# Kernel optimization log

Measured on AMD Instinct MI355X. Metric: run time of the kernel, lower is better.

Reference implementation:

```python
import jax, jax.numpy as jnp
import numpy as np

N = 8192
NFEAT = 512
NHID = 512
NCLASS = 8
EPS = 1e-9
ADJ_P = 0.01  # edge density


def setup_inputs() -> dict:
    key = jax.random.key(0)
    ks = jax.random.split(key, 16)
    adj = (jax.random.uniform(ks[0], (N, N)) < ADJ_P).astype(jnp.float32)
    x = jax.random.normal(ks[1], (N, NFEAT), dtype=jnp.float32)
    s_in = 1.0 / np.sqrt(NFEAT)
    s_h = 1.0 / np.sqrt(NHID)
    return {
        "adj": adj,
        "x": x,
        "gcn1_W": jax.random.normal(ks[2], (NFEAT, NHID), jnp.float32) * s_in,
        "gcn1_b": jnp.zeros((NHID,), jnp.float32),
        "Qw": jax.random.normal(ks[3], (NHID, NHID), jnp.float32) * s_h,
        "Qb": jnp.zeros((NHID,), jnp.float32),
        "Kw": jax.random.normal(ks[4], (NHID, NHID), jnp.float32) * s_h,
        "Kb": jnp.zeros((NHID,), jnp.float32),
        "Vw": jax.random.normal(ks[5], (NHID, NHID), jnp.float32) * s_h,
        "Vb": jnp.zeros((NHID,), jnp.float32),
        "ln_g": jnp.ones((NHID,), jnp.float32),
        "ln_b": jnp.zeros((NHID,), jnp.float32),
        "gcn2_W": jax.random.normal(ks[6], (NHID, NCLASS), jnp.float32) * s_h,
        "gcn2_b": jnp.zeros((NCLASS,), jnp.float32),
    }


def _gcn_norm(a):
    # symmetric degree normalization D^{-1/2} A D^{-1/2}, degrees = row sums
    d_inv_sqrt = jax.lax.rsqrt(a.sum(axis=1) + EPS)  # [N]
    return d_inv_sqrt[:, None] * a * d_inv_sqrt[None, :]


def _layer_norm(x, g, b):
    mu = x.mean(axis=-1, keepdims=True)
    var = x.var(axis=-1, keepdims=True)
    return (x - mu) * jax.lax.rsqrt(var + 1e-5) * g + b


def reference(adj, x, gcn1_W, gcn1_b, Qw, Qb, Kw, Kb, Vw, Vb, ln_g, ln_b, gcn2_W, gcn2_b):
    # GraphConvolution: adj @ (x W) + b, then ReLU
    h = jax.nn.relu(adj @ (x @ gcn1_W) + gcn1_b)  # [N, NHID]
    Qh = h @ Qw + Qb
    Kh = h @ Kw + Kb
    Vh = h @ Vw + Vb
    # adjacency-masked dense scores (multiplicative mask, as in original)
    A_tilde = adj * (Qh @ Kh.T)  # [N, N]
    attention = jax.nn.softmax(A_tilde, axis=1)
    X_tilde = _gcn_norm(attention) @ Vh  # [N, NHID]
    X_tilde = _layer_norm(X_tilde, ln_g, ln_b)
    z = adj @ (X_tilde @ gcn2_W) + gcn2_b  # [N, NCLASS]
    return jax.nn.softmax(z, axis=1)
```

## Files before the change

kernel.cpp:

```cpp
#include <hip/hip_runtime.h>
#include <math.h>

#define N_NODES 8192
#define NFEAT 512
#define NHID 512
#define NCLASS 8
#define RCAP 192
#define KB_SPLIT 1536
#define KA_SPLIT 1024
#define CANDCAP 64
#define FILTER_MARGIN 96.0f

__device__ inline ushort f2bf(float f) {
  uint32_t u = __float_as_uint(f);
  uint32_t r = u + 0x7fffu + ((u >> 16) & 1u);
  return (ushort)(r >> 16);
}
__device__ inline float bf2f(ushort h) { return __uint_as_float(((uint32_t)h) << 16); }

__global__ __launch_bounds__(256) void build_ell(const float* __restrict__ adj,
                                                 int* __restrict__ colidx,
                                                 int* __restrict__ deg) {
  int row = blockIdx.x;
  __shared__ int cnt;
  __shared__ int cols[RCAP];
  if (threadIdx.x == 0) cnt = 0;
  __syncthreads();
  const float4* arow = (const float4*)(adj + (size_t)row * N_NODES);
  for (int i = threadIdx.x; i < N_NODES / 4; i += 256) {
    float4 v = arow[i];
    int base = i * 4;
    if (v.x > 0.5f) { int p = atomicAdd(&cnt, 1); if (p < RCAP) cols[p] = base; }
    if (v.y > 0.5f) { int p = atomicAdd(&cnt, 1); if (p < RCAP) cols[p] = base + 1; }
    if (v.z > 0.5f) { int p = atomicAdd(&cnt, 1); if (p < RCAP) cols[p] = base + 2; }
    if (v.w > 0.5f) { int p = atomicAdd(&cnt, 1); if (p < RCAP) cols[p] = base + 3; }
  }
  __syncthreads();
  int d = cnt < RCAP ? cnt : RCAP;
  if (threadIdx.x == 0) deg[row] = d;
  for (int i = threadIdx.x; i < d; i += 256) colidx[(size_t)row * RCAP + i] = cols[i];
}

__global__ void transpose512(const float* __restrict__ in, float* __restrict__ out) {
  __shared__ float tile[32][33];
  int x = blockIdx.x * 32 + threadIdx.x;
  int y0 = blockIdx.y * 32;
  for (int i = threadIdx.y; i < 32; i += 8)
    tile[i][threadIdx.x] = in[(size_t)(y0 + i) * 512 + x];
  __syncthreads();
  int xo = blockIdx.y * 32 + threadIdx.x;
  int yo0 = blockIdx.x * 32;
  for (int i = threadIdx.y; i < 32; i += 8)
    out[(size_t)(yo0 + i) * 512 + xo] = tile[threadIdx.x][i];
}

__global__ __launch_bounds__(256) void sgemm64x128(const float* __restrict__ A,
                                                   const float* __restrict__ B,
                                                   float* __restrict__ C,
                                                   int M, int Nn, int K, int ldc) {
  __shared__ float As[16][68];
  __shared__ float Bs[16][132];
  const int tid = threadIdx.x;
  const int bm = blockIdx.y * 64, bn = blockIdx.x * 128;
  const int tx = tid & 15, ty = tid >> 4;
  const int arow = tid >> 2, acol = (tid & 3) << 2;
  const int brow = tid >> 4, bcol = (tid & 15) << 2;
  float acc[4][8];
#pragma unroll
  for (int i = 0; i < 4; ++i)
#pragma unroll
    for (int j = 0; j < 8; ++j) acc[i][j] = 0.f;
  const float* Ap = A + (size_t)(bm + arow) * K + acol;
  const float* Bp = B + (size_t)brow * Nn + bn + bcol;
// ... 169 lines not shown
    }
    if (Tsum && col >= 512) {
      csum += __shfl_xor(csum, 16, 64);
      csum += __shfl_xor(csum, 32, 64);
      if (q == 0) atomicAdd(&Tsum[col - 512], csum);
    }
  }
}

__global__ __launch_bounds__(64) void bias_prep(const float* __restrict__ Qw, const float* __restrict__ Kw,
                                                const float* __restrict__ Qb, const float* __restrict__ Kb,
                                                float* __restrict__ u, float* __restrict__ w,
                                                float* __restrict__ cbuf) {
  int k = blockIdx.x;
  int lane = threadIdx.x;
  if (k == NHID) {
    float s = 0.f;
    for (int j = lane; j < NHID; j += 64) s = fmaf(Qb[j], Kb[j], s);
#pragma unroll
    for (int o = 32; o > 0; o >>= 1) s += __shfl_down(s, o, 64);
    if (lane == 0) cbuf[0] = s;
    return;
  }
  float su = 0.f, sw = 0.f;
  for (int j = lane; j < NHID; j += 64) {
    su = fmaf(Qw[(size_t)k * NHID + j], Kb[j], su);
    sw = fmaf(Kw[(size_t)k * NHID + j], Qb[j], sw);
  }
#pragma unroll
  for (int o = 32; o > 0; o >>= 1) { su += __shfl_down(su, o, 64); sw += __shfl_down(sw, o, 64); }
  if (lane == 0) { u[k] = su; w[k] = sw; }
}

__global__ __launch_bounds__(128) void spmm_fused(const float* __restrict__ xW,
                                                  const int* __restrict__ colidx,
                                                  const int* __restrict__ deg,
                                                  const float* __restrict__ b1,
                                                  const float* __restrict__ u, const float* __restrict__ w,
                                                  float* __restrict__ h, ushort* __restrict__ Hs,
                                                  float* __restrict__ a_vec, float* __restrict__ b_vec) {
  __shared__ int scols[RCAP];
  __shared__ float ra[2], rb[2];
  int row = blockIdx.x, t = threadIdx.x;
  int d = deg[row];
  for (int i = t; i < d; i += 128) scols[i] = colidx[(size_t)row * RCAP + i];
  __syncthreads();
  float4 acc = make_float4(0.f, 0.f, 0.f, 0.f);
  int e = 0;
  for (; e + 8 <= d; e += 8) {
    float4 v0 = ((const float4*)(xW + (size_t)scols[e + 0] * NHID))[t];
    float4 v1 = ((const float4*)(xW + (size_t)scols[e + 1] * NHID))[t];
    float4 v2 = ((const float4*)(xW + (size_t)scols[e + 2] * NHID))[t];
    float4 v3 = ((const float4*)(xW + (size_t)scols[e + 3] * NHID))[t];
    float4 v4 = ((const float4*)(xW + (size_t)scols[e + 4] * NHID))[t];
    float4 v5 = ((const float4*)(xW + (size_t)scols[e + 5] * NHID))[t];
    float4 v6 = ((const float4*)(xW + (size_t)scols[e + 6] * NHID))[t];
    float4 v7 = ((const float4*)(xW + (size_t)scols[e + 7] * NHID))[t];
    acc.x += ((v0.x + v1.x) + (v2.x + v3.x)) + ((v4.x + v5.x) + (v6.x + v7.x));
    acc.y += ((v0.y + v1.y) + (v2.y + v3.y)) + ((v4.y + v5.y) + (v6.y + v7.y));
    acc.z += ((v0.z + v1.z) + (v2.z + v3.z)) + ((v4.z + v5.z) + (v6.z + v7.z));
    acc.w += ((v0.w + v1.w) + (v2.w + v3.w)) + ((v4.w + v5.w) + (v6.w + v7.w));
  }
  for (; e < d; ++e) {
    float4 v = ((const float4*)(xW + (size_t)scols[e] * NHID))[t];
    acc.x += v.x; acc.y += v.y; acc.z += v.z; acc.w += v.w;
  }
  float4 bv = ((const float4*)b1)[t];
  float4 o = make_float4(fmaxf(acc.x + bv.x, 0.f), fmaxf(acc.y + bv.y, 0.f),
                         fmaxf(acc.z + bv.z, 0.f), fmaxf(acc.w + bv.w, 0.f));
  ((float4*)(h + (size_t)row * NHID))[t] = o;
  ushort4 hi, lo;
  hi.x = f2bf(o.x); hi.y = f2bf(o.y); hi.z = f2bf(o.z); hi.w = f2bf(o.w);
  lo.x = f2bf(o.x - bf2f(hi.x)); lo.y = f2bf(o.y - bf2f(hi.y));
  lo.z = f2bf(o.z - bf2f(hi.z)); lo.w = f2bf(o.w - bf2f(hi.w));
  ushort* hr = Hs + (size_t)row * KA_SPLIT;
  ((ushort4*)hr)[t] = hi;
  ((ushort4*)(hr + 512))[t] = lo;
  float4 uv = ((const float4*)u)[t], wv4 = ((const float4*)w)[t];
  float sa = fmaf(o.x, uv.x, fmaf(o.y, uv.y, fmaf(o.z, uv.z, o.w * uv.w)));
  float sb = fmaf(o.x, wv4.x, fmaf(o.y, wv4.y, fmaf(o.z, wv4.z, o.w * wv4.w)));
  int wv = t >> 6, lane = t & 63;
#pragma unroll
  for (int off = 32; off > 0; off >>= 1) { sa += __shfl_down(sa, off, 64); sb += __shfl_down(sb, off, 64); }
  if (lane == 0) { ra[wv] = sa; rb[wv] = sb; }
  __syncthreads();
  if (t == 0) { a_vec[row] = ra[0] + ra[1]; b_vec[row] = rb[0] + rb[1]; }
}

__global__ __launch_bounds__(256) void score2_agg_ln(
    const float* __restrict__ G, int ldg, const float* __restrict__ h,
    const ushort* __restrict__ Hs, const int* __restrict__ colidx, const int* __restrict__ deg,
    const float* __restrict__ a_vec, const float* __restrict__ b_vec,
    const float* __restrict__ cbuf, const float* __restrict__ Vh, int ldv,
    const float* __restrict__ T, const float* __restrict__ lng,
    const float* __restrict__ lnb, float* __restrict__ Xt) {
  __shared__ int scols[4][RCAP];
  __shared__ float sbv[4][RCAP];
  __shared__ float sv[4][RCAP];
  __shared__ int cand[4][CANDCAP];
  __shared__ int ccnt[4];
  int t = threadIdx.x, wv = t >> 6, lane = t & 63;
  int row = blockIdx.x * 4 + wv;
  int d = deg[row];
  int q = lane >> 4, u = lane & 15;
  if (lane == 0) ccnt[wv] = 0;
  float4 ga4[4][2];
  const float4* Gr4 = (const float4*)(G + (size_t)row * ldg);
#pragma unroll
  for (int it2 = 0; it2 < 4; ++it2) {
    ga4[it2][0] = Gr4[it2 * 32 + 2 * u];
    ga4[it2][1] = Gr4[it2 * 32 + 2 * u + 1];
  }
  for (int i = lane; i < d; i += 64) {
    int c = colidx[(size_t)row * RCAP + i];
    scols[wv][i] = c;
    sbv[wv][i] = b_vec[c];
  }
  __syncthreads();
  for (int e0 = 0; e0 < d; e0 += 4) {
    int e = e0 + q;
    bool act = e < d;
    int col = scols[wv][act ? e : 0];
    const uint4* hr = (const uint4*)(Hs + (size_t)col * KA_SPLIT);
    float s_a = 0.f, s_b = 0.f;
#pragma unroll
    for (int it2 = 0; it2 < 4; ++it2) {
      uint4 p = hr[it2 * 16 + u];
      float4 g0 = ga4[it2][0], g1 = ga4[it2][1];
      s_a = fmaf(__uint_as_float(p.x << 16), g0.x, s_a);
      s_a = fmaf(__uint_as_float(p.x & 0xffff0000u), g0.y, s_a);
      s_a = fmaf(__uint_as_float(p.y << 16), g0.z, s_a);
      s_a = fmaf(__uint_as_float(p.y & 0xffff0000u), g0.w, s_a);
      s_b = fmaf(__uint_as_float(p.z << 16), g1.x, s_b);
      s_b = fmaf(__uint_as_float(p.z & 0xffff0000u), g1.y, s_b);
      s_b = fmaf(__uint_as_float(p.w << 16), g1.z, s_b);
      s_b = fmaf(__uint_as_float(p.w & 0xffff0000u), g1.w, s_b);
    }
    float s = s_a + s_b;
    s += __shfl_down(s, 8, 16);
    s += __shfl_down(s, 4, 16);
    s += __shfl_down(s, 2, 16);
    s += __shfl_down(s, 1, 16);
    if (u == 0 && act) sv[wv][e] = s + sbv[wv][e];
  }
  __syncthreads();
  float fm = -1e30f;
  for (int i = lane; i < d; i += 64) fm = fmaxf(fm, sv[wv][i]);
#pragma unroll
  for (int o = 32; o > 0; o >>= 1) fm = fmaxf(fm, __shfl_xor(fm, o, 64));
  for (int i = lane; i < d; i += 64) {
    if (sv[wv][i] >= fm - FILTER_MARGIN) {
      int p = atomicAdd(&ccnt[wv], 1);
      if (p < CANDCAP) cand[wv][p] = i;
    }
  }
  __syncthreads();
  int nc = ccnt[wv];
  bool ovf = nc > CANDCAP;
  if (ovf) nc = d;
  float ai = a_vec[row] + cbuf[0];
  for (int c0 = 0; c0 < nc; c0 += 4) {
    int idx = c0 + q;
    bool act = idx < nc;
    int e = act ? (ovf ? idx : cand[wv][idx]) : 0;
    int col = scols[wv][e];
    const float4* hr = (const float4*)(h + (size_t)col * NHID);
    float s_a = 0.f, s_b = 0.f;
#pragma unroll
    for (int it2 = 0; it2 < 4; ++it2) {
      float4 h0 = hr[it2 * 32 + 2 * u], h1 = hr[it2 * 32 + 2 * u + 1];
      float4 g0 = ga4[it2][0], g1 = ga4[it2][1];
      s_a = fmaf(h0.x, g0.x, s_a); s_a = fmaf(h0.y, g0.y, s_a);
      s_a = fmaf(h0.z, g0.z, s_a); s_a = fmaf(h0.w, g0.w, s_a);
      s_b = fmaf(h1.x, g1.x, s_b); s_b = fmaf(h1.y, g1.y, s_b);
      s_b = fmaf(h1.z, g1.z, s_b); s_b = fmaf(h1.w, g1.w, s_b);
    }
    float s = s_a + s_b;
    s += __shfl_down(s, 8, 16);
    s += __shfl_down(s, 4, 16);
    s += __shfl_down(s, 2, 16);
    s += __shfl_down(s, 1, 16);
    if (u == 0 && act) sv[wv][e] = s + ai + sbv[wv][e];
  }
  __syncthreads();
  float m = 0.f;
  for (int i = lane; i < nc; i += 64) {
    int e = ovf ? i : cand[wv][i];
    m = fmaxf(m, sv[wv][e]);
  }
#pragma unroll
  for (int o = 32; o > 0; o >>= 1) m = fmaxf(m, __shfl_xor(m, o, 64));
  float ssum = 0.f;
  for (int i = lane; i < nc; i += 64) {
    int e = ovf ? i : cand[wv][i];
    float ex = expf(sv[wv][e] - m);
    sv[wv][e] = ex;
    ssum += ex;
  }
#pragma unroll
  for (int o = 32; o > 0; o >>= 1) ssum += __shfl_xor(ssum, o, 64);
  float em = expf(-m);
  float inv = 1.f / (ssum + (float)(N_NODES - d) * em);
  float ci = em * inv;
  __syncthreads();
  float4 a0 = make_float4(0.f, 0.f, 0.f, 0.f), a1 = a0;
  for (int i = 0; i < nc; ++i) {
    int e = ovf ? i : cand[wv][i];
    float we = sv[wv][e] * inv;
    if (we > 1e-12f) {
      const float4* vr = (const float4*)(Vh + (size_t)scols[wv][e] * ldv);
      float4 v0 = vr[lane * 2], v1 = vr[lane * 2 + 1];
      a0.x = fmaf(we, v0.x, a0.x); a0.y = fmaf(we, v0.y, a0.y);
      a0.z = fmaf(we, v0.z, a0.z); a0.w = fmaf(we, v0.w, a0.w);
      a1.x = fmaf(we, v1.x, a1.x); a1.y = fmaf(we, v1.y, a1.y);
      a1.z = fmaf(we, v1.z, a1.z); a1.w = fmaf(we, v1.w, a1.w);
    }
  }
  float4 t0 = ((const float4*)T)[lane * 2], t1 = ((const float4*)T)[lane * 2 + 1];
  a0.x = fmaf(ci, t0.x, a0.x); a0.y = fmaf(ci, t0.y, a0.y);
  a0.z = fmaf(ci, t0.z, a0.z); a0.w = fmaf(ci, t0.w, a0.w);
  a1.x = fmaf(ci, t1.x, a1.x); a1.y = fmaf(ci, t1.y, a1.y);
  a1.z = fmaf(ci, t1.z, a1.z); a1.w = fmaf(ci, t1.w, a1.w);
  float s1 = ((a0.x + a0.y) + (a0.z + a0.w)) + ((a1.x + a1.y) + (a1.z + a1.w));
  float s2 = ((a0.x * a0.x + a0.y * a0.y) + (a0.z * a0.z + a0.w * a0.w)) +
             ((a1.x * a1.x + a1.y * a1.y) + (a1.z * a1.z + a1.w * a1.w));
#pragma unroll
  for (int o = 32; o > 0; o >>= 1) { s1 += __shfl_xor(s1, o, 64); s2 += __shfl_xor(s2, o, 64); }
  float mu = s1 * (1.f / NHID);
  float var = s2 * (1.f / NHID) - mu * mu;
  float rstd = rsqrtf(var + 1e-5f);
  float4 g0 = ((const float4*)lng)[lane * 2], g1 = ((const float4*)lng)[lane * 2 + 1];
  float4 b0 = ((const float4*)lnb)[lane * 2], b1 = ((const float4*)lnb)[lane * 2 + 1];
  float4 o0, o1;
  o0.x = (a0.x - mu) * rstd * g0.x + b0.x;
  o0.y = (a0.y - mu) * rstd * g0.y + b0.y;
  o0.z = (a0.z - mu) * rstd * g0.z + b0.z;
  o0.w = (a0.w - mu) * rstd * g0.w + b0.w;
  o1.x = (a1.x - mu) * rstd * g1.x + b1.x;
  o1.y = (a1.y - mu) * rstd * g1.y + b1.y;
  o1.z = (a1.z - mu) * rstd * g1.z + b1.z;
  o1.w = (a1.w - mu) * rstd * g1.w + b1.w;
  float4* xr = (float4*)(Xt + (size_t)row * NHID);
  xr[lane * 2] = o0;
  xr[lane * 2 + 1] = o1;
}

__global__ __launch_bounds__(256) void xt_w2(const float* __restrict__ Xt, const float* __restrict__ W2,
                                             float* __restrict__ Y) {
  __shared__ float w2s[NHID * NCLASS];
  int t = threadIdx.x;
  for (int i = t; i < NHID * NCLASS; i += 256) w2s[i] = W2[i];
  __syncthreads();
  int wv = t >> 6, lane = t & 63;
  int row = blockIdx.x * 4 + wv;
  const float4* xr = (const float4*)(Xt + (size_t)row * NHID);
  float4 x0 = xr[lane * 2], x1 = xr[lane * 2 + 1];
  float xv[8] = {x0.x, x0.y, x0.z, x0.w, x1.x, x1.y, x1.z, x1.w};
  float acc[NCLASS];
#pragma unroll
  for (int c = 0; c < NCLASS; ++c) acc[c] = 0.f;
#pragma unroll
  for (int kk = 0; kk < 8; ++kk) {
    int k = lane * 8 + kk;
#pragma unroll
    for (int c = 0; c < NCLASS; ++c) acc[c] = fmaf(xv[kk], w2s[k * NCLASS + c], acc[c]);
  }
#pragma unroll
  for (int c = 0; c < NCLASS; ++c)
#pragma unroll
    for (int o = 32; o > 0; o >>= 1) acc[c] += __shfl_down(acc[c], o, 64);
  if (lane == 0) {
    *(float4*)(Y + (size_t)row * NCLASS) = make_float4(acc[0], acc[1], acc[2], acc[3]);
    *(float4*)(Y + (size_t)row * NCLASS + 4) = make_float4(acc[4], acc[5], acc[6], acc[7]);
  }
}

__global__ __launch_bounds__(256) void final_spmm_softmax(const float* __restrict__ Y,
                                                          const int* __restrict__ colidx,
                                                          const int* __restrict__ deg,
                                                          const float* __restrict__ b2,
                                                          float* __restrict__ out) {
  int t = threadIdx.x;
  int wv = t >> 6, lane = t & 63;
  int row = blockIdx.x * 4 + wv;
  int d = deg[row];
  const int* cols = colidx + (size_t)row * RCAP;
  float acc[8];
#pragma unroll
  for (int c = 0; c < 8; ++c) acc[c] = 0.f;
  for (int e = lane; e < d; e += 64) {
    int col = cols[e];
    const float4* yr = (const float4*)(Y + (size_t)col * 8);
    float4 y0 = yr[0], y1 = yr[1];
    acc[0] += y0.x; acc[1] += y0.y; acc[2] += y0.z; acc[3] += y0.w;
    acc[4] += y1.x; acc[5] += y1.y; acc[6] += y1.z; acc[7] += y1.w;
  }
#pragma unroll
  for (int c = 0; c < 8; ++c)
#pragma unroll
    for (int o = 32; o > 0; o >>= 1) acc[c] += __shfl_down(acc[c], o, 64);
  if (lane == 0) {
    float z[8];
    float m = -1e30f;
#pragma unroll
    for (int c = 0; c < 8; ++c) { z[c] = acc[c] + b2[c]; m = fmaxf(m, z[c]); }
    float s = 0.f;
#pragma unroll
    for (int c = 0; c < 8; ++c) { z[c] = expf(z[c] - m); s += z[c]; }
    float inv = 1.f / s;
    *(float4*)(out + (size_t)row * 8) = make_float4(z[0] * inv, z[1] * inv, z[2] * inv, z[3] * inv);
    *(float4*)(out + (size_t)row * 8 + 4) = make_float4(z[4] * inv, z[5] * inv, z[6] * inv, z[7] * inv);
  }
}

extern "C" void kernel_launch(void* const* d_in, const int* in_sizes, int n_in,
                              void* d_out, int out_size, void* d_ws, size_t ws_size,
                              hipStream_t stream) {
  const float* adj = (const float*)d_in[0];
  const float* x = (const float*)d_in[1];
  const float* W1 = (const float*)d_in[2];
  const float* b1 = (const float*)d_in[3];
  const float* Qw = (const float*)d_in[4];
  const float* Qb = (const float*)d_in[5];
  const float* Kw = (const float*)d_in[6];
  const float* Kb = (const float*)d_in[7];
  const float* Vw = (const float*)d_in[8];
  const float* Vb = (const float*)d_in[9];
  const float* ln_g = (const float*)d_in[10];
  const float* ln_b = (const float*)d_in[11];
  const float* W2 = (const float*)d_in[12];
  const float* b2 = (const float*)d_in[13];
  float* out = (float*)d_out;

  char* ws = (char*)d_ws;
  size_t off = 0;
  auto alloc = [&](size_t bytes) -> void* {
    void* p = ws + off;
    off = (off + bytes + 255) & ~(size_t)255;
    return p;
  };
  int* colidx = (int*)alloc((size_t)N_NODES * RCAP * 4);
  int* deg = (int*)alloc((size_t)N_NODES * 4);
  float* bufA = (float*)alloc((size_t)N_NODES * NHID * 4);
  float* bufB = (float*)alloc((size_t)N_NODES * NHID * 4);
  float* GVh = (float*)alloc((size_t)N_NODES * 1024 * 4);
  ushort* Xs = (ushort*)alloc((size_t)N_NODES * KA_SPLIT * 2);
  ushort* Hs = (ushort*)alloc((size_t)N_NODES * KA_SPLIT * 2);
  ushort* W1ts = (ushort*)alloc((size_t)512 * KB_SPLIT * 2);
  ushort* Bcts = (ushort*)alloc((size_t)1024 * KB_SPLIT * 2);
  float* KwT = (float*)alloc((size_t)512 * 512 * 4);
  float* Mmat = (float*)alloc((size_t)512 * 512 * 4);
  float* bcat = (float*)alloc((size_t)1024 * 4);
  float* a_vec = (float*)alloc((size_t)N_NODES * 4);
  float* b_vec = (float*)alloc((size_t)N_NODES * 4);
  float* u_vec = (float*)alloc((size_t)NHID * 4);
  float* w_vec = (float*)alloc((size_t)NHID * 4);
  float* cbuf = (float*)alloc(256);
  float* T = (float*)alloc((size_t)NHID * 4);
  float* Y = (float*)alloc((size_t)N_NODES * NCLASS * 4);
  (void)in_sizes; (void)n_in; (void)out_size; (void)ws_size;

  build_ell<<<N_NODES, 256, 0, stream>>>(adj, colidx, deg);
  transpose512<<<dim3(16, 16), dim3(32, 8), 0, stream>>>(Kw, KwT);
  bias_prep<<<NHID + 1, 64, 0, stream>>>(Qw, Kw, Qb, Kb, u_vec, w_vec, cbuf);
  sgemm64x128<<<dim3(4, 8), 256, 0, stream>>>(Qw, KwT, Mmat, 512, 512, 512, 512);
  split_a2<<<(N_NODES * 128) / 256, 256, 0, stream>>>(x, Xs);
  split_bt<<<(512 * 384) / 256, 256, 0, stream>>>(W1, W1ts, 512);
  mfma_gemm_bt<<<dim3(4, 64), 256, 0, stream>>>(Xs, W1ts, nullptr, bufA, 512, nullptr);
  spmm_fused<<<N_NODES, 128, 0, stream>>>(bufA, colidx, deg, b1, u_vec, w_vec, bufB, Hs, a_vec, b_vec);
  split_bt_cat<<<(1024 * 384) / 256, 256, 0, stream>>>(Mmat, Vw, Bcts);
  prep_misc<<<6, 256, 0, stream>>>(Vb, bcat, T);
  mfma_gemm_bt<<<dim3(8, 64), 256, 0, stream>>>(Hs, Bcts, bcat, GVh, 1024, T);
  score2_agg_ln<<<N_NODES / 4, 256, 0, stream>>>(GVh, 1024, bufB, Hs, colidx, deg, a_vec, b_vec,
                                                 cbuf, GVh + 512, 1024, T, ln_g, ln_b, bufA);
  xt_w2<<<N_NODES / 4, 256, 0, stream>>>(bufA, W2, Y);
  final_spmm_softmax<<<N_NODES / 4, 256, 0, stream>>>(Y, colidx, deg, b2, out);
}
```

Before: 763.5 us.

## Segment ELL columns into four column-range passes for cache locality; fuse W2 projection

Splits each row's neighbor list into four column segments of 2048 nodes, then runs the SpMM and the bf16 score filter as four passes, one segment each. Every pass only gathers rows from a 2048-node window, so the gathered working set can stay cache-resident. The xt_w2 kernel is folded into the attention/layernorm kernel, which also removes the Xt round-trip. Costs are more kernel launches, partial-sum read/write of h across the passes, a new score buffer, and a fixed 64-per-segment cap that can drop edges on dense segments.

```diff
diff --git a/kernel.cpp b/kernel.cpp
--- a/kernel.cpp
+++ b/kernel.cpp
@@ -5,7 +5,10 @@
 #define NFEAT 512
 #define NHID 512
 #define NCLASS 8
-#define RCAP 192
+#define NSEG 4
+#define SEGW 2048
+#define SEGCAP 64
+#define SLOTS 256
 #define KB_SPLIT 1536
 #define KA_SPLIT 1024
 #define CANDCAP 64
@@ -20,25 +23,30 @@
 
 __global__ __launch_bounds__(256) void build_ell(const float* __restrict__ adj,
                                                  int* __restrict__ colidx,
-                                                 int* __restrict__ deg) {
+                                                 int* __restrict__ deg4) {
   int row = blockIdx.x;
-  __shared__ int cnt;
-  __shared__ int cols[RCAP];
-  if (threadIdx.x == 0) cnt = 0;
+  __shared__ int cnt[NSEG];
+  __shared__ int cols[NSEG][SEGCAP];
+  if (threadIdx.x < NSEG) cnt[threadIdx.x] = 0;
   __syncthreads();
   const float4* arow = (const float4*)(adj + (size_t)row * N_NODES);
   for (int i = threadIdx.x; i < N_NODES / 4; i += 256) {
     float4 v = arow[i];
     int base = i * 4;
-    if (v.x > 0.5f) { int p = atomicAdd(&cnt, 1); if (p < RCAP) cols[p] = base; }
-    if (v.y > 0.5f) { int p = atomicAdd(&cnt, 1); if (p < RCAP) cols[p] = base + 1; }
-    if (v.z > 0.5f) { int p = atomicAdd(&cnt, 1); if (p < RCAP) cols[p] = base + 2; }
-    if (v.w > 0.5f) { int p = atomicAdd(&cnt, 1); if (p < RCAP) cols[p] = base + 3; }
-  }
-  __syncthreads();
-  int d = cnt < RCAP ? cnt : RCAP;
-  if (threadIdx.x == 0) deg[row] = d;
-  for (int i = threadIdx.x; i < d; i += 256) colidx[(size_t)row * RCAP + i] = cols[i];
+    if (v.x > 0.5f) { int c = base + 0, s = c >> 11; int p = atomicAdd(&cnt[s], 1); if (p < SEGCAP) cols[s][p] = c; }
+    if (v.y > 0.5f) { int c = base + 1, s = c >> 11; int p = atomicAdd(&cnt[s], 1); if (p < SEGCAP) cols[s][p] = c; }
+    if (v.z > 0.5f) { int c = base + 2, s = c >> 11; int p = atomicAdd(&cnt[s], 1); if (p < SEGCAP) cols[s][p] = c; }
+    if (v.w > 0.5f) { int c = base + 3, s = c >> 11; int p = atomicAdd(&cnt[s], 1); if (p < SEGCAP) cols[s][p] = c; }
+  }
+  __syncthreads();
+  if (threadIdx.x < NSEG) {
+    int c = cnt[threadIdx.x];
+    deg4[row * NSEG + threadIdx.x] = c < SEGCAP ? c : SEGCAP;
+  }
+  for (int s = 0; s < NSEG; ++s) {
+    int d = cnt[s] < SEGCAP ? cnt[s] : SEGCAP;
+    for (int i = threadIdx.x; i < d; i += 256) colidx[(size_t)row * SLOTS + s * SEGCAP + i] = cols[s][i];
+  }
 }
 
 __global__ void transpose512(const float* __restrict__ in, float* __restrict__ out) {
@@ -274,38 +282,42 @@
   if (lane == 0) { u[k] = su; w[k] = sw; }
 }
 
-__global__ __launch_bounds__(128) void spmm_fused(const float* __restrict__ xW,
-                                                  const int* __restrict__ colidx,
-                                                  const int* __restrict__ deg,
-                                                  const float* __restrict__ b1,
-                                                  const float* __restrict__ u, const float* __restrict__ w,
-                                                  float* __restrict__ h, ushort* __restrict__ Hs,
-                                                  float* __restrict__ a_vec, float* __restrict__ b_vec) {
-  __shared__ int scols[RCAP];
+__global__ __launch_bounds__(128) void spmm_pass(const float* __restrict__ xW,
+                                                 const int* __restrict__ colidx,
+                                                 const int* __restrict__ deg4, int seg,
+                                                 const float* __restrict__ b1,
+                                                 const float* __restrict__ u_vec,
+                                                 const float* __restrict__ w_vec,
+                                                 float* __restrict__ h, ushort* __restrict__ Hs,
+                                                 float* __restrict__ a_vec, float* __restrict__ b_vec,
+                                                 int isFinal) {
+  __shared__ int scols[SEGCAP];
   __shared__ float ra[2], rb[2];
   int row = blockIdx.x, t = threadIdx.x;
-  int d = deg[row];
-  for (int i = t; i < d; i += 128) scols[i] = colidx[(size_t)row * RCAP + i];
-  __syncthreads();
-  float4 acc = make_float4(0.f, 0.f, 0.f, 0.f);
+  int d = deg4[row * NSEG + seg];
+  for (int i = t; i < d; i += 128) scols[i] = colidx[(size_t)row * SLOTS + seg * SEGCAP + i];
+  __syncthreads();
+  float4 acc;
+  if (seg == 0) acc = make_float4(0.f, 0.f, 0.f, 0.f);
+  else acc = ((const float4*)(h + (size_t)row * NHID))[t];
   int e = 0;
-  for (; e + 8 <= d; e += 8) {
+  for (; e + 4 <= d; e += 4) {
     float4 v0 = ((const float4*)(xW + (size_t)scols[e + 0] * NHID))[t];
     float4 v1 = ((const float4*)(xW + (size_t)scols[e + 1] * NHID))[t];
     float4 v2 = ((const float4*)(xW + (size_t)scols[e + 2] * NHID))[t];
     float4 v3 = ((const float4*)(xW + (size_t)scols[e + 3] * NHID))[t];
-    float4 v4 = ((const float4*)(xW + (size_t)scols[e + 4] * NHID))[t];
-    float4 v5 = ((const float4*)(xW + (size_t)scols[e + 5] * NHID))[t];
-    float4 v6 = ((const float4*)(xW + (size_t)scols[e + 6] * NHID))[t];
-    float4 v7 = ((const float4*)(xW + (size_t)scols[e + 7] * NHID))[t];
-    acc.x += ((v0.x + v1.x) + (v2.x + v3.x)) + ((v4.x + v5.x) + (v6.x + v7.x));
-    acc.y += ((v0.y + v1.y) + (v2.y + v3.y)) + ((v4.y + v5.y) + (v6.y + v7.y));
-    acc.z += ((v0.z + v1.z) + (v2.z + v3.z)) + ((v4.z + v5.z) + (v6.z + v7.z));
-    acc.w += ((v0.w + v1.w) + (v2.w + v3.w)) + ((v4.w + v5.w) + (v6.w + v7.w));
+    acc.x += (v0.x + v1.x) + (v2.x + v3.x);
+    acc.y += (v0.y + v1.y) + (v2.y + v3.y);
+    acc.z += (v0.z + v1.z) + (v2.z + v3.z);
+    acc.w += (v0.w + v1.w) + (v2.w + v3.w);
   }
   for (; e < d; ++e) {
     float4 v = ((const float4*)(xW + (size_t)scols[e] * NHID))[t];
     acc.x += v.x; acc.y += v.y; acc.z += v.z; acc.w += v.w;
+  }
+  if (!isFinal) {
+    ((float4*)(h + (size_t)row * NHID))[t] = acc;
+    return;
   }
   float4 bv = ((const float4*)b1)[t];
   float4 o = make_float4(fmaxf(acc.x + bv.x, 0.f), fmaxf(acc.y + bv.y, 0.f),
@@ -318,34 +330,27 @@
   ushort* hr = Hs + (size_t)row * KA_SPLIT;
   ((ushort4*)hr)[t] = hi;
   ((ushort4*)(hr + 512))[t] = lo;
-  float4 uv = ((const float4*)u)[t], wv4 = ((const float4*)w)[t];
+  float4 uv = ((const float4*)u_vec)[t], wv4 = ((const float4*)w_vec)[t];
   float sa = fmaf(o.x, uv.x, fmaf(o.y, uv.y, fmaf(o.z, uv.z, o.w * uv.w)));
   float sb = fmaf(o.x, wv4.x, fmaf(o.y, wv4.y, fmaf(o.z, wv4.z, o.w * wv4.w)));
-  int wv = t >> 6, lane = t & 63;
+  int wid = t >> 6, lane = t & 63;
 #pragma unroll
   for (int off = 32; off > 0; off >>= 1) { sa += __shfl_down(sa, off, 64); sb += __shfl_down(sb, off, 64); }
-  if (lane == 0) { ra[wv] = sa; rb[wv] = sb; }
+  if (lane == 0) { ra[wid] = sa; rb[wid] = sb; }
   __syncthreads();
   if (t == 0) { a_vec[row] = ra[0] + ra[1]; b_vec[row] = rb[0] + rb[1]; }
 }
 
-__global__ __launch_bounds__(256) void score2_agg_ln(
-    const float* __restrict__ G, int ldg, const float* __restrict__ h,
-    const ushort* __restrict__ Hs, const int* __restrict__ colidx, const int* __restrict__ deg,
-    const float* __restrict__ a_vec, const float* __restrict__ b_vec,
-    const float* __restrict__ cbuf, const float* __restrict__ Vh, int ldv,
-    const float* __restrict__ T, const float* __restrict__ lng,
-    const float* __restrict__ lnb, float* __restrict__ Xt) {
-  __shared__ int scols[4][RCAP];
-  __shared__ float sbv[4][RCAP];
-  __shared__ float sv[4][RCAP];
-  __shared__ int cand[4][CANDCAP];
-  __shared__ int ccnt[4];
+__global__ __launch_bounds__(256) void filter_pass(const float* __restrict__ G, int ldg,
+                                                   const ushort* __restrict__ Hs,
+                                                   const int* __restrict__ colidx,
+                                                   const int* __restrict__ deg4,
+                                                   const float* __restrict__ b_vec,
+                                                   float* __restrict__ svg, int seg) {
   int t = threadIdx.x, wv = t >> 6, lane = t & 63;
   int row = blockIdx.x * 4 + wv;
-  int d = deg[row];
   int q = lane >> 4, u = lane & 15;
-  if (lane == 0) ccnt[wv] = 0;
+  int d = deg4[row * NSEG + seg];
   float4 ga4[4][2];
   const float4* Gr4 = (const float4*)(G + (size_t)row * ldg);
 #pragma unroll
@@ -353,16 +358,12 @@
     ga4[it2][0] = Gr4[it2 * 32 + 2 * u];
     ga4[it2][1] = Gr4[it2 * 32 + 2 * u + 1];
   }
-  for (int i = lane; i < d; i += 64) {
-    int c = colidx[(size_t)row * RCAP + i];
-    scols[wv][i] = c;
-    sbv[wv][i] = b_vec[c];
-  }
-  __syncthreads();
+  const int* ci = colidx + (size_t)row * SLOTS + seg * SEGCAP;
+  float* so = svg + (size_t)row * SLOTS + seg * SEGCAP;
   for (int e0 = 0; e0 < d; e0 += 4) {
     int e = e0 + q;
     bool act = e < d;
-    int col = scols[wv][act ? e : 0];
+    int col = ci[act ? e : 0];
     const uint4* hr = (const uint4*)(Hs + (size_t)col * KA_SPLIT);
     float s_a = 0.f, s_b = 0.f;
 #pragma unroll
@@ -383,15 +384,56 @@
     s += __shfl_down(s, 4, 16);
     s += __shfl_down(s, 2, 16);
     s += __shfl_down(s, 1, 16);
-    if (u == 0 && act) sv[wv][e] = s + sbv[wv][e];
+    if (u == 0 && act) so[e] = s + b_vec[col];
+  }
+}
+
+__global__ __launch_bounds__(256) void score2_main(
+    const float* __restrict__ G, int ldg, const float* __restrict__ h,
+    const int* __restrict__ colidx, const int* __restrict__ deg4,
+    const float* __restrict__ a_vec, const float* __restrict__ b_vec,
+    const float* __restrict__ cbuf, const float* __restrict__ Vh, int ldv,
+    const float* __restrict__ svg, const float* __restrict__ T,
+    const float* __restrict__ lng, const float* __restrict__ lnb,
+    const float* __restrict__ W2, float* __restrict__ Y) {
+  __shared__ int scols[4][SLOTS];
+  __shared__ float sf[4][SLOTS];
+  __shared__ int cand[4][CANDCAP];
+  __shared__ int ccnt[4];
+  __shared__ float w2s[NHID * NCLASS];
+  int t = threadIdx.x, wv = t >> 6, lane = t & 63;
+  int row = blockIdx.x * 4 + wv;
+  int q = lane >> 4, u = lane & 15;
+  for (int i = t; i < NHID * NCLASS; i += 256) w2s[i] = W2[i];
+  if (lane == 0) ccnt[wv] = 0;
+  int4 dv = ((const int4*)deg4)[row];
+  int dtot = dv.x + dv.y + dv.z + dv.w;
+  for (int i = lane; i < SLOTS; i += 64) {
+    int s = i >> 6, k = i & 63;
+    int ds = (s == 0) ? dv.x : (s == 1) ? dv.y : (s == 2) ? dv.z : dv.w;
+    int c = 0;
+    float f = -1e30f;
+    if (k < ds) {
+      c = colidx[(size_t)row * SLOTS + i];
+      f = svg[(size_t)row * SLOTS + i];
+    }
+    scols[wv][i] = c;
+    sf[wv][i] = f;
+  }
+  float4 ga4[4][2];
+  const float4* Gr4 = (const float4*)(G + (size_t)row * ldg);
+#pragma unroll
+  for (int it2 = 0; it2 < 4; ++it2) {
+    ga4[it2][0] = Gr4[it2 * 32 + 2 * u];
+    ga4[it2][1] = Gr4[it2 * 32 + 2 * u + 1];
   }
   __syncthreads();
   float fm = -1e30f;
-  for (int i = lane; i < d; i += 64) fm = fmaxf(fm, sv[wv][i]);
+  for (int i = lane; i < SLOTS; i += 64) fm = fmaxf(fm, sf[wv][i]);
 #pragma unroll
   for (int o = 32; o > 0; o >>= 1) fm = fmaxf(fm, __shfl_xor(fm, o, 64));
-  for (int i = lane; i < d; i += 64) {
-    if (sv[wv][i] >= fm - FILTER_MARGIN) {
+  for (int i = lane; i < SLOTS; i += 64) {
+    if (sf[wv][i] >= fm - FILTER_MARGIN) {
       int p = atomicAdd(&ccnt[wv], 1);
       if (p < CANDCAP) cand[wv][p] = i;
     }
@@ -399,13 +441,14 @@
   __syncthreads();
   int nc = ccnt[wv];
   bool ovf = nc > CANDCAP;
-  if (ovf) nc = d;
+  if (ovf) nc = SLOTS;
   float ai = a_vec[row] + cbuf[0];
   for (int c0 = 0; c0 < nc; c0 += 4) {
     int idx = c0 + q;
     bool act = idx < nc;
-    int e = act ? (ovf ? idx : cand[wv][idx]) : 0;
-    int col = scols[wv][e];
+    int slot = act ? (ovf ? idx : cand[wv][idx]) : 0;
+    if (ovf && act) act = sf[wv][slot] > -1e29f;
+    int col = scols[wv][slot];
     const float4* hr = (const float4*)(h + (size_t)col * NHID);
     float s_a = 0.f, s_b = 0.f;
 #pragma unroll
@@ -422,35 +465,35 @@
     s += __shfl_down(s, 4, 16);
     s += __shfl_down(s, 2, 16);
     s += __shfl_down(s, 1, 16);
-    if (u == 0 && act) sv[wv][e] = s + ai + sbv[wv][e];
+    if (u == 0 && act) sf[wv][slot] = s + ai + b_vec[col];
   }
   __syncthreads();
   float m = 0.f;
   for (int i = lane; i < nc; i += 64) {
-    int e = ovf ? i : cand[wv][i];
-    m = fmaxf(m, sv[wv][e]);
+    int slot = ovf ? i : cand[wv][i];
+    m = fmaxf(m, sf[wv][slot]);
   }
 #pragma unroll
   for (int o = 32; o > 0; o >>= 1) m = fmaxf(m, __shfl_xor(m, o, 64));
   float ssum = 0.f;
   for (int i = lane; i < nc; i += 64) {
-    int e = ovf ? i : cand[wv][i];
-    float ex = expf(sv[wv][e] - m);
-    sv[wv][e] = ex;
+    int slot = ovf ? i : cand[wv][i];
+    float ex = expf(sf[wv][slot] - m);
+    sf[wv][slot] = ex;
     ssum += ex;
   }
 #pragma unroll
   for (int o = 32; o > 0; o >>= 1) ssum += __shfl_xor(ssum, o, 64);
   float em = expf(-m);
-  float inv = 1.f / (ssum + (float)(N_NODES - d) * em);
+  float inv = 1.f / (ssum + (float)(N_NODES - dtot) * em);
   float ci = em * inv;
   __syncthreads();
   float4 a0 = make_float4(0.f, 0.f, 0.f, 0.f), a1 = a0;
   for (int i = 0; i < nc; ++i) {
-    int e = ovf ? i : cand[wv][i];
-    float we = sv[wv][e] * inv;
+    int slot = ovf ? i : cand[wv][i];
+    float we = sf[wv][slot] * inv;
     if (we > 1e-12f) {
-      const float4* vr = (const float4*)(Vh + (size_t)scols[wv][e] * ldv);
+      const float4* vr = (const float4*)(Vh + (size_t)scols[wv][slot] * ldv);
       float4 v0 = vr[lane * 2], v1 = vr[lane * 2 + 1];
       a0.x = fmaf(we, v0.x, a0.x); a0.y = fmaf(we, v0.y, a0.y);
       a0.z = fmaf(we, v0.z, a0.z); a0.w = fmaf(we, v0.w, a0.w);
@@ -472,70 +515,58 @@
   float var = s2 * (1.f / NHID) - mu * mu;
   float rstd = rsqrtf(var + 1e-5f);
   float4 g0 = ((const float4*)lng)[lane * 2], g1 = ((const float4*)lng)[lane * 2 + 1];
-  float4 b0 = ((const float4*)lnb)[lane * 2], b1 = ((const float4*)lnb)[lane * 2 + 1];
+  float4 b0 = ((const float4*)lnb)[lane * 2], b1v = ((const float4*)lnb)[lane * 2 + 1];
   float4 o0, o1;
   o0.x = (a0.x - mu) * rstd * g0.x + b0.x;
   o0.y = (a0.y - mu) * rstd * g0.y + b0.y;
   o0.z = (a0.z - mu) * rstd * g0.z + b0.z;
   o0.w = (a0.w - mu) * rstd * g0.w + b0.w;
-  o1.x = (a1.x - mu) * rstd * g1.x + b1.x;
-  o1.y = (a1.y - mu) * rstd * g1.y + b1.y;
-  o1.z = (a1.z - mu) * rstd * g1.z + b1.z;
-  o1.w = (a1.w - mu) * rstd * g1.w + b1.w;
-  float4* xr = (float4*)(Xt + (size_t)row * NHID);
-  xr[lane * 2] = o0;
-  xr[lane * 2 + 1] = o1;
-}
-
-__global__ __launch_bounds__(256) void xt_w2(const float* __restrict__ Xt, const float* __restrict__ W2,
-                                             float* __restrict__ Y) {
-  __shared__ float w2s[NHID * NCLASS];
-  int t = threadIdx.x;
-  for (int i = t; i < NHID * NCLASS; i += 256) w2s[i] = W2[i];
-  __syncthreads();
-  int wv = t >> 6, lane = t & 63;
-  int row = blockIdx.x * 4 + wv;
-  const float4* xr = (const float4*)(Xt + (size_t)row * NHID);
-  float4 x0 = xr[lane * 2], x1 = xr[lane * 2 + 1];
-  float xv[8] = {x0.x, x0.y, x0.z, x0.w, x1.x, x1.y, x1.z, x1.w};
-  float acc[NCLASS];
-#pragma unroll
-  for (int c = 0; c < NCLASS; ++c) acc[c] = 0.f;
+  o1.x = (a1.x - mu) * rstd * g1.x + b1v.x;
+  o1.y = (a1.y - mu) * rstd * g1.y + b1v.y;
+  o1.z = (a1.z - mu) * rstd * g1.z + b1v.z;
+  o1.w = (a1.w - mu) * rstd * g1.w + b1v.w;
+  float xv[8] = {o0.x, o0.y, o0.z, o0.w, o1.x, o1.y, o1.z, o1.w};
+  float accc[NCLASS];
+#pragma unroll
+  for (int c = 0; c < NCLASS; ++c) accc[c] = 0.f;
 #pragma unroll
   for (int kk = 0; kk < 8; ++kk) {
     int k = lane * 8 + kk;
 #pragma unroll
-    for (int c = 0; c < NCLASS; ++c) acc[c] = fmaf(xv[kk], w2s[k * NCLASS + c], acc[c]);
+    for (int c = 0; c < NCLASS; ++c) accc[c] = fmaf(xv[kk], w2s[k * NCLASS + c], accc[c]);
   }
 #pragma unroll
   for (int c = 0; c < NCLASS; ++c)
 #pragma unroll
-    for (int o = 32; o > 0; o >>= 1) acc[c] += __shfl_down(acc[c], o, 64);
+    for (int o = 32; o > 0; o >>= 1) accc[c] += __shfl_down(accc[c], o, 64);
   if (lane == 0) {
-    *(float4*)(Y + (size_t)row * NCLASS) = make_float4(acc[0], acc[1], acc[2], acc[3]);
-    *(float4*)(Y + (size_t)row * NCLASS + 4) = make_float4(acc[4], acc[5], acc[6], acc[7]);
+    *(float4*)(Y + (size_t)row * NCLASS) = make_float4(accc[0], accc[1], accc[2], accc[3]);
+    *(float4*)(Y + (size_t)row * NCLASS + 4) = make_float4(accc[4], accc[5], accc[6], accc[7]);
   }
 }
 
 __global__ __launch_bounds__(256) void final_spmm_softmax(const float* __restrict__ Y,
                                                           const int* __restrict__ colidx,
-                                                          const int* __restrict__ deg,
+                                                          const int* __restrict__ deg4,
                                                           const float* __restrict__ b2,
                                                           float* __restrict__ out) {
   int t = threadIdx.x;
   int wv = t >> 6, lane = t & 63;
   int row = blockIdx.x * 4 + wv;
-  int d = deg[row];
-  const int* cols = colidx + (size_t)row * RCAP;
+  int4 dv = ((const int4*)deg4)[row];
   float acc[8];
 #pragma unroll
   for (int c = 0; c < 8; ++c) acc[c] = 0.f;
-  for (int e = lane; e < d; e += 64) {
-    int col = cols[e];
-    const float4* yr = (const float4*)(Y + (size_t)col * 8);
-    float4 y0 = yr[0], y1 = yr[1];
-    acc[0] += y0.x; acc[1] += y0.y; acc[2] += y0.z; acc[3] += y0.w;
-    acc[4] += y1.x; acc[5] += y1.y; acc[6] += y1.z; acc[7] += y1.w;
+  for (int i = lane; i < SLOTS; i += 64) {
+    int s = i >> 6, k = i & 63;
+    int ds = (s == 0) ? dv.x : (s == 1) ? dv.y : (s == 2) ? dv.z : dv.w;
+    if (k < ds) {
+      int col = colidx[(size_t)row * SLOTS + i];
+      const float4* yr = (const float4*)(Y + (size_t)col * 8);
+      float4 y0 = yr[0], y1 = yr[1];
+      acc[0] += y0.x; acc[1] += y0.y; acc[2] += y0.z; acc[3] += y0.w;
+      acc[4] += y1.x; acc[5] += y1.y; acc[6] += y1.z; acc[7] += y1.w;
+    }
   }
 #pragma unroll
   for (int c = 0; c < 8; ++c)
@@ -581,11 +612,12 @@
     off = (off + bytes + 255) & ~(size_t)255;
     return p;
   };
-  int* colidx = (int*)alloc((size_t)N_NODES * RCAP * 4);
-  int* deg = (int*)alloc((size_t)N_NODES * 4);
+  int* colidx = (int*)alloc((size_t)N_NODES * SLOTS * 4);
+  int* deg4 = (int*)alloc((size_t)N_NODES * NSEG * 4);
   float* bufA = (float*)alloc((size_t)N_NODES * NHID * 4);
   float* bufB = (float*)alloc((size_t)N_NODES * NHID * 4);
   float* GVh = (float*)alloc((size_t)N_NODES * 1024 * 4);
+  float* svg = (float*)alloc((size_t)N_NODES * SLOTS * 4);
   ushort* Xs = (ushort*)alloc((size_t)N_NODES * KA_SPLIT * 2);
   ushort* Hs = (ushort*)alloc((size_t)N_NODES * KA_SPLIT * 2);
   ushort* W1ts = (ushort*)alloc((size_t)512 * KB_SPLIT * 2);
@@ -602,19 +634,22 @@
   float* Y = (float*)alloc((size_t)N_NODES * NCLASS * 4);
   (void)in_sizes; (void)n_in; (void)out_size; (void)ws_size;
 
-  build_ell<<<N_NODES, 256, 0, stream>>>(adj, colidx, deg);
+  build_ell<<<N_NODES, 256, 0, stream>>>(adj, colidx, deg4);
   transpose512<<<dim3(16, 16), dim3(32, 8), 0, stream>>>(Kw, KwT);
   bias_prep<<<NHID + 1, 64, 0, stream>>>(Qw, Kw, Qb, Kb, u_vec, w_vec, cbuf);
   sgemm64x128<<<dim3(4, 8), 256, 0, stream>>>(Qw, KwT, Mmat, 512, 512, 512, 512);
   split_a2<<<(N_NODES * 128) / 256, 256, 0, stream>>>(x, Xs);
   split_bt<<<(512 * 384) / 256, 256, 0, stream>>>(W1, W1ts, 512);
   mfma_gemm_bt<<<dim3(4, 64), 256, 0, stream>>>(Xs, W1ts, nullptr, bufA, 512, nullptr);
-  spmm_fused<<<N_NODES, 128, 0, stream>>>(bufA, colidx, deg, b1, u_vec, w_vec, bufB, Hs, a_vec, b_vec);
+  for (int s = 0; s < NSEG; ++s)
+    spmm_pass<<<N_NODES, 128, 0, stream>>>(bufA, colidx, deg4, s, b1, u_vec, w_vec,
+                                           bufB, Hs, a_vec, b_vec, s == NSEG - 1);
   split_bt_cat<<<(1024 * 384) / 256, 256, 0, stream>>>(Mmat, Vw, Bcts);
   prep_misc<<<6, 256, 0, stream>>>(Vb, bcat, T);
   mfma_gemm_bt<<<dim3(8, 64), 256, 0, stream>>>(Hs, Bcts, bcat, GVh, 1024, T);
-  score2_agg_ln<<<N_NODES / 4, 256, 0, stream>>>(GVh, 1024, bufB, Hs, colidx, deg, a_vec, b_vec,
-                                                 cbuf, GVh + 512, 1024, T, ln_g, ln_b, bufA);
-  xt_w2<<<N_NODES / 4, 256, 0, stream>>>(bufA, W2, Y);
-  final_spmm_softmax<<<N_NODES / 4, 256, 0, stream>>>(Y, colidx, deg, b2, out);
-}
+  for (int s = 0; s < NSEG; ++s)
+    filter_pass<<<N_NODES / 4, 256, 0, stream>>>(GVh, 1024, Hs, colidx, deg4, b_vec, svg, s);
+  score2_main<<<N_NODES / 4, 256, 0, stream>>>(GVh, 1024, bufB, colidx, deg4, a_vec, b_vec,
+                                               cbuf, GVh + 512, 1024, svg, T, ln_g, ln_b, W2, Y);
+  final_spmm_softmax<<<N_NODES / 4, 256, 0, stream>>>(Y, colidx, deg4, b2, out);
+}
```

Result: faster. 747.3 us (-2.1%).

## Fuse Xt·W2 into aggregation kernel and batch SpMM rows per block

Applied to the files above, without the earlier changes.

The layer-norm output is multiplied by W2 inside score2_agg_ln, which removes the xt_w2 kernel and the round trip of the full Xt matrix through global memory. The first SpMM now handles 8 rows per block and interleaves their neighbour gathers to expose more memory-level parallelism, at the cost of more registers and shared memory. build_ell's row scan is unrolled with a barrier per iteration. The extra W2 staging adds shared memory to the aggregation kernel, which may lower its occupancy.

```diff
diff --git a/kernel.cpp b/kernel.cpp
--- a/kernel.cpp
+++ b/kernel.cpp
@@ -10,6 +10,7 @@
 #define KA_SPLIT 1024
 #define CANDCAP 64
 #define FILTER_MARGIN 96.0f
+#define SROWS 8
 
 __device__ inline ushort f2bf(float f) {
   uint32_t u = __float_as_uint(f);
@@ -27,15 +28,17 @@
   if (threadIdx.x == 0) cnt = 0;
   __syncthreads();
   const float4* arow = (const float4*)(adj + (size_t)row * N_NODES);
-  for (int i = threadIdx.x; i < N_NODES / 4; i += 256) {
+#pragma unroll
+  for (int it = 0; it < N_NODES / 4 / 256; ++it) {
+    int i = it * 256 + threadIdx.x;
     float4 v = arow[i];
     int base = i * 4;
     if (v.x > 0.5f) { int p = atomicAdd(&cnt, 1); if (p < RCAP) cols[p] = base; }
     if (v.y > 0.5f) { int p = atomicAdd(&cnt, 1); if (p < RCAP) cols[p] = base + 1; }
     if (v.z > 0.5f) { int p = atomicAdd(&cnt, 1); if (p < RCAP) cols[p] = base + 2; }
     if (v.w > 0.5f) { int p = atomicAdd(&cnt, 1); if (p < RCAP) cols[p] = base + 3; }
-  }
-  __syncthreads();
+    __syncthreads();
+  }
   int d = cnt < RCAP ? cnt : RCAP;
   if (threadIdx.x == 0) deg[row] = d;
   for (int i = threadIdx.x; i < d; i += 256) colidx[(size_t)row * RCAP + i] = cols[i];
@@ -274,59 +277,63 @@
   if (lane == 0) { u[k] = su; w[k] = sw; }
 }
 
-__global__ __launch_bounds__(128) void spmm_fused(const float* __restrict__ xW,
-                                                  const int* __restrict__ colidx,
-                                                  const int* __restrict__ deg,
-                                                  const float* __restrict__ b1,
-                                                  const float* __restrict__ u, const float* __restrict__ w,
-                                                  float* __restrict__ h, ushort* __restrict__ Hs,
-                                                  float* __restrict__ a_vec, float* __restrict__ b_vec) {
-  __shared__ int scols[RCAP];
+__global__ __launch_bounds__(128) void spmm_persist(const float* __restrict__ xW,
+                                                    const int* __restrict__ colidx,
+                                                    const int* __restrict__ deg,
+                                                    const float* __restrict__ b1,
+                                                    const float* __restrict__ u, const float* __restrict__ w,
+                                                    float* __restrict__ h, ushort* __restrict__ Hs,
+                                                    float* __restrict__ a_vec, float* __restrict__ b_vec) {
+  __shared__ int scols[SROWS][RCAP];
   __shared__ float ra[2], rb[2];
-  int row = blockIdx.x, t = threadIdx.x;
-  int d = deg[row];
-  for (int i = t; i < d; i += 128) scols[i] = colidx[(size_t)row * RCAP + i];
-  __syncthreads();
-  float4 acc = make_float4(0.f, 0.f, 0.f, 0.f);
-  int e = 0;
-  for (; e + 8 <= d; e += 8) {
-    float4 v0 = ((const float4*)(xW + (size_t)scols[e + 0] * NHID))[t];
-    float4 v1 = ((const float4*)(xW + (size_t)scols[e + 1] * NHID))[t];
-    float4 v2 = ((const float4*)(xW + (size_t)scols[e + 2] * NHID))[t];
-    float4 v3 = ((const float4*)(xW + (size_t)scols[e + 3] * NHID))[t];
-    float4 v4 = ((const float4*)(xW + (size_t)scols[e + 4] * NHID))[t];
-    float4 v5 = ((const float4*)(xW + (size_t)scols[e + 5] * NHID))[t];
-    float4 v6 = ((const float4*)(xW + (size_t)scols[e + 6] * NHID))[t];
-    float4 v7 = ((const float4*)(xW + (size_t)scols[e + 7] * NHID))[t];
-    acc.x += ((v0.x + v1.x) + (v2.x + v3.x)) + ((v4.x + v5.x) + (v6.x + v7.x));
-    acc.y += ((v0.y + v1.y) + (v2.y + v3.y)) + ((v4.y + v5.y) + (v6.y + v7.y));
-    acc.z += ((v0.z + v1.z) + (v2.z + v3.z)) + ((v4.z + v5.z) + (v6.z + v7.z));
-    acc.w += ((v0.w + v1.w) + (v2.w + v3.w)) + ((v4.w + v5.w) + (v6.w + v7.w));
-  }
-  for (; e < d; ++e) {
-    float4 v = ((const float4*)(xW + (size_t)scols[e] * NHID))[t];
-    acc.x += v.x; acc.y += v.y; acc.z += v.z; acc.w += v.w;
+  int t = threadIdx.x;
+  int row0 = blockIdx.x * SROWS;
+  int d[SROWS];
+  int maxd = 0;
+#pragma unroll
+  for (int r = 0; r < SROWS; ++r) {
+    d[r] = deg[row0 + r];
+    maxd = max(maxd, d[r]);
+    for (int i = t; i < d[r]; i += 128) scols[r][i] = colidx[(size_t)(row0 + r) * RCAP + i];
+  }
+  __syncthreads();
+  float4 acc[SROWS];
+#pragma unroll
+  for (int r = 0; r < SROWS; ++r) acc[r] = make_float4(0.f, 0.f, 0.f, 0.f);
+  for (int k = 0; k < maxd; ++k) {
+#pragma unroll
+    for (int r = 0; r < SROWS; ++r) {
+      if (k < d[r]) {
+        float4 v = ((const float4*)(xW + (size_t)scols[r][k] * NHID))[t];
+        acc[r].x += v.x; acc[r].y += v.y; acc[r].z += v.z; acc[r].w += v.w;
+      }
+    }
   }
   float4 bv = ((const float4*)b1)[t];
-  float4 o = make_float4(fmaxf(acc.x + bv.x, 0.f), fmaxf(acc.y + bv.y, 0.f),
-                         fmaxf(acc.z + bv.z, 0.f), fmaxf(acc.w + bv.w, 0.f));
-  ((float4*)(h + (size_t)row * NHID))[t] = o;
-  ushort4 hi, lo;
-  hi.x = f2bf(o.x); hi.y = f2bf(o.y); hi.z = f2bf(o.z); hi.w = f2bf(o.w);
-  lo.x = f2bf(o.x - bf2f(hi.x)); lo.y = f2bf(o.y - bf2f(hi.y));
-  lo.z = f2bf(o.z - bf2f(hi.z)); lo.w = f2bf(o.w - bf2f(hi.w));
-  ushort* hr = Hs + (size_t)row * KA_SPLIT;
-  ((ushort4*)hr)[t] = hi;
-  ((ushort4*)(hr + 512))[t] = lo;
   float4 uv = ((const float4*)u)[t], wv4 = ((const float4*)w)[t];
-  float sa = fmaf(o.x, uv.x, fmaf(o.y, uv.y, fmaf(o.z, uv.z, o.w * uv.w)));
-  float sb = fmaf(o.x, wv4.x, fmaf(o.y, wv4.y, fmaf(o.z, wv4.z, o.w * wv4.w)));
-  int wv = t >> 6, lane = t & 63;
-#pragma unroll
-  for (int off = 32; off > 0; off >>= 1) { sa += __shfl_down(sa, off, 64); sb += __shfl_down(sb, off, 64); }
-  if (lane == 0) { ra[wv] = sa; rb[wv] = sb; }
-  __syncthreads();
-  if (t == 0) { a_vec[row] = ra[0] + ra[1]; b_vec[row] = rb[0] + rb[1]; }
+  int wid = t >> 6, lane = t & 63;
+#pragma unroll
+  for (int r = 0; r < SROWS; ++r) {
+    int row = row0 + r;
+    float4 o = make_float4(fmaxf(acc[r].x + bv.x, 0.f), fmaxf(acc[r].y + bv.y, 0.f),
+                           fmaxf(acc[r].z + bv.z, 0.f), fmaxf(acc[r].w + bv.w, 0.f));
+    ((float4*)(h + (size_t)row * NHID))[t] = o;
+    ushort4 hi, lo;
+    hi.x = f2bf(o.x); hi.y = f2bf(o.y); hi.z = f2bf(o.z); hi.w = f2bf(o.w);
+    lo.x = f2bf(o.x - bf2f(hi.x)); lo.y = f2bf(o.y - bf2f(hi.y));
+    lo.z = f2bf(o.z - bf2f(hi.z)); lo.w = f2bf(o.w - bf2f(hi.w));
+    ushort* hr = Hs + (size_t)row * KA_SPLIT;
+    ((ushort4*)hr)[t] = hi;
+    ((ushort4*)(hr + 512))[t] = lo;
+    float sa = fmaf(o.x, uv.x, fmaf(o.y, uv.y, fmaf(o.z, uv.z, o.w * uv.w)));
+    float sb = fmaf(o.x, wv4.x, fmaf(o.y, wv4.y, fmaf(o.z, wv4.z, o.w * wv4.w)));
+#pragma unroll
+    for (int off = 32; off > 0; off >>= 1) { sa += __shfl_down(sa, off, 64); sb += __shfl_down(sb, off, 64); }
+    if (lane == 0) { ra[wid] = sa; rb[wid] = sb; }
+    __syncthreads();
+    if (t == 0) { a_vec[row] = ra[0] + ra[1]; b_vec[row] = rb[0] + rb[1]; }
+    __syncthreads();
+  }
 }
 
 __global__ __launch_bounds__(256) void score2_agg_ln(
@@ -335,16 +342,18 @@
     const float* __restrict__ a_vec, const float* __restrict__ b_vec,
     const float* __restrict__ cbuf, const float* __restrict__ Vh, int ldv,
     const float* __restrict__ T, const float* __restrict__ lng,
-    const float* __restrict__ lnb, float* __restrict__ Xt) {
+    const float* __restrict__ lnb, const float* __restrict__ W2, float* __restrict__ Y) {
   __shared__ int scols[4][RCAP];
   __shared__ float sbv[4][RCAP];
   __shared__ float sv[4][RCAP];
   __shared__ int cand[4][CANDCAP];
   __shared__ int ccnt[4];
+  __shared__ float w2s[NHID * NCLASS];
   int t = threadIdx.x, wv = t >> 6, lane = t & 63;
   int row = blockIdx.x * 4 + wv;
   int d = deg[row];
   int q = lane >> 4, u = lane & 15;
+  for (int i = t; i < NHID * NCLASS; i += 256) w2s[i] = W2[i];
   if (lane == 0) ccnt[wv] = 0;
   float4 ga4[4][2];
   const float4* Gr4 = (const float4*)(G + (size_t)row * ldg);
@@ -472,48 +481,33 @@
   float var = s2 * (1.f / NHID) - mu * mu;
   float rstd = rsqrtf(var + 1e-5f);
   float4 g0 = ((const float4*)lng)[lane * 2], g1 = ((const float4*)lng)[lane * 2 + 1];
-  float4 b0 = ((const float4*)lnb)[lane * 2], b1 = ((const float4*)lnb)[lane * 2 + 1];
+  float4 b0 = ((const float4*)lnb)[lane * 2], b1v = ((const float4*)lnb)[lane * 2 + 1];
   float4 o0, o1;
   o0.x = (a0.x - mu) * rstd * g0.x + b0.x;
   o0.y = (a0.y - mu) * rstd * g0.y + b0.y;
   o0.z = (a0.z - mu) * rstd * g0.z + b0.z;
   o0.w = (a0.w - mu) * rstd * g0.w + b0.w;
-  o1.x = (a1.x - mu) * rstd * g1.x + b1.x;
-  o1.y = (a1.y - mu) * rstd * g1.y + b1.y;
-  o1.z = (a1.z - mu) * rstd * g1.z + b1.z;
-  o1.w = (a1.w - mu) * rstd * g1.w + b1.w;
-  float4* xr = (float4*)(Xt + (size_t)row * NHID);
-  xr[lane * 2] = o0;
-  xr[lane * 2 + 1] = o1;
-}
-
-__global__ __launch_bounds__(256) void xt_w2(const float* __restrict__ Xt, const float* __restrict__ W2,
-                                             float* __restrict__ Y) {
-  __shared__ float w2s[NHID * NCLASS];
-  int t = threadIdx.x;
-  for (int i = t; i < NHID * NCLASS; i += 256) w2s[i] = W2[i];
-  __syncthreads();
-  int wv = t >> 6, lane = t & 63;
-  int row = blockIdx.x * 4 + wv;
-  const float4* xr = (const float4*)(Xt + (size_t)row * NHID);
-  float4 x0 = xr[lane * 2], x1 = xr[lane * 2 + 1];
-  float xv[8] = {x0.x, x0.y, x0.z, x0.w, x1.x, x1.y, x1.z, x1.w};
-  float acc[NCLASS];
-#pragma unroll
-  for (int c = 0; c < NCLASS; ++c) acc[c] = 0.f;
+  o1.x = (a1.x - mu) * rstd * g1.x + b1v.x;
+  o1.y = (a1.y - mu) * rstd * g1.y + b1v.y;
+  o1.z = (a1.z - mu) * rstd * g1.z + b1v.z;
+  o1.w = (a1.w - mu) * rstd * g1.w + b1v.w;
+  float xv[8] = {o0.x, o0.y, o0.z, o0.w, o1.x, o1.y, o1.z, o1.w};
+  float accc[NCLASS];
+#pragma unroll
+  for (int c = 0; c < NCLASS; ++c) accc[c] = 0.f;
 #pragma unroll
   for (int kk = 0; kk < 8; ++kk) {
     int k = lane * 8 + kk;
 #pragma unroll
-    for (int c = 0; c < NCLASS; ++c) acc[c] = fmaf(xv[kk], w2s[k * NCLASS + c], acc[c]);
+    for (int c = 0; c < NCLASS; ++c) accc[c] = fmaf(xv[kk], w2s[k * NCLASS + c], accc[c]);
   }
 #pragma unroll
   for (int c = 0; c < NCLASS; ++c)
 #pragma unroll
-    for (int o = 32; o > 0; o >>= 1) acc[c] += __shfl_down(acc[c], o, 64);
+    for (int o = 32; o > 0; o >>= 1) accc[c] += __shfl_down(accc[c], o, 64);
   if (lane == 0) {
-    *(float4*)(Y + (size_t)row * NCLASS) = make_float4(acc[0], acc[1], acc[2], acc[3]);
-    *(float4*)(Y + (size_t)row * NCLASS + 4) = make_float4(acc[4], acc[5], acc[6], acc[7]);
+    *(float4*)(Y + (size_t)row * NCLASS) = make_float4(accc[0], accc[1], accc[2], accc[3]);
+    *(float4*)(Y + (size_t)row * NCLASS + 4) = make_float4(accc[4], accc[5], accc[6], accc[7]);
   }
 }
 
@@ -609,12 +603,12 @@
   split_a2<<<(N_NODES * 128) / 256, 256, 0, stream>>>(x, Xs);
   split_bt<<<(512 * 384) / 256, 256, 0, stream>>>(W1, W1ts, 512);
   mfma_gemm_bt<<<dim3(4, 64), 256, 0, stream>>>(Xs, W1ts, nullptr, bufA, 512, nullptr);
-  spmm_fused<<<N_NODES, 128, 0, stream>>>(bufA, colidx, deg, b1, u_vec, w_vec, bufB, Hs, a_vec, b_vec);
+  spmm_persist<<<N_NODES / SROWS, 128, 0, stream>>>(bufA, colidx, deg, b1, u_vec, w_vec,
+                                                    bufB, Hs, a_vec, b_vec);
   split_bt_cat<<<(1024 * 384) / 256, 256, 0, stream>>>(Mmat, Vw, Bcts);
   prep_misc<<<6, 256, 0, stream>>>(Vb, bcat, T);
   mfma_gemm_bt<<<dim3(8, 64), 256, 0, stream>>>(Hs, Bcts, bcat, GVh, 1024, T);
   score2_agg_ln<<<N_NODES / 4, 256, 0, stream>>>(GVh, 1024, bufB, Hs, colidx, deg, a_vec, b_vec,
-                                                 cbuf, GVh + 512, 1024, T, ln_g, ln_b, bufA);
-  xt_w2<<<N_NODES / 4, 256, 0, stream>>>(bufA, W2, Y);
+                                                 cbuf, GVh + 512, 1024, T, ln_g, ln_b, W2, Y);
   final_spmm_softmax<<<N_NODES / 4, 256, 0, stream>>>(Y, colidx, deg, b2, out);
 }
```

Result: slower. 800.4 us (+4.8%).
